# Kernel tuning notes

Measured on AMD Instinct MI355X. Metric: run time of the kernel, lower is better.

## Reference

```python
import jax, jax.numpy as jnp
import numpy as np

N, M, D = 8192, 8192, 64


def setup_inputs() -> dict:
    key = jax.random.key(0)
    kx, ky = jax.random.split(key)
    X = jax.random.normal(kx, (N, D), dtype=jnp.float32)
    Y = jax.random.normal(ky, (M, D), dtype=jnp.float32)
    return {"X": X, "Y": Y}


def reference(X, Y):
    # Pairwise Euclidean distances via the |x|^2 + |y|^2 - 2<x,y> identity
    # (avoids materializing the [N, M, D] difference tensor).
    x2 = jnp.sum(X * X, axis=1)[:, None]          # [N, 1]
    y2 = jnp.sum(Y * Y, axis=1)[None, :]          # [1, M]
    d2 = x2 + y2 - 2.0 * (X @ Y.T)                # [N, M]
    d = jnp.sqrt(jnp.maximum(d2, 0.0))            # Euclidean distance matrix
    dis_1 = jnp.mean(jnp.min(d, axis=1))          # avg over X of nearest-in-Y
    dis_2 = jnp.mean(jnp.min(d, axis=0))          # avg over Y of nearest-in-X
    return dis_1 + dis_2
```

## Files before the change

### kernel.cpp

```cpp
#include <hip/hip_runtime.h>
#include <math.h>


#define NROWS 8192
#define DDIM  64
#define CHUNKS 8
#define LSTR 72

typedef __bf16 bf16_t;
typedef bf16_t bf16x8 __attribute__((ext_vector_type(8)));
typedef float  f32x4  __attribute__((ext_vector_type(4)));


__global__ __launch_bounds__(256, 2)
void mine_kernel(const float* __restrict__ X, const float* __restrict__ Y,
                 float* __restrict__ rslab, float* __restrict__ cslab,
                 float* __restrict__ out) {
  __shared__ bf16_t Ys[128 * LSTR];
  __shared__ float y2s[128];

  const int tid = threadIdx.x;
  const int L = tid & 63;
  const int w = tid >> 6;
  const int lr = L & 15;
  const int q  = L >> 4;
  const int rh = w >> 1, ch = w & 1;
  const int itile = blockIdx.x & 63;
  const int slice = blockIdx.x >> 6;
  const int i0 = itile * 128;
  const int rgb = rh * 64, cgb = ch * 64;
  const int jbase = slice * (CHUNKS * 128);

  if (blockIdx.x == 0 && tid == 0) out[0] = 0.f;

  bf16x8 Af[8];
  float x2r[16];
  {
    float x2acc[4];
#pragma unroll
    for (int a = 0; a < 4; ++a) {
      const float4* rp = (const float4*)(X + (i0 + rgb + a * 16 + lr) * DDIM);
      float4 u0 = rp[q * 2],     u1 = rp[q * 2 + 1];
      float4 u2 = rp[8 + q * 2], u3 = rp[8 + q * 2 + 1];
      float s = 0.f;
      s = fmaf(u0.x, u0.x, s); s = fmaf(u0.y, u0.y, s);
      s = fmaf(u0.z, u0.z, s); s = fmaf(u0.w, u0.w, s);
      s = fmaf(u1.x, u1.x, s); s = fmaf(u1.y, u1.y, s);
      s = fmaf(u1.z, u1.z, s); s = fmaf(u1.w, u1.w, s);
      s = fmaf(u2.x, u2.x, s); s = fmaf(u2.y, u2.y, s);
      s = fmaf(u2.z, u2.z, s); s = fmaf(u2.w, u2.w, s);
      s = fmaf(u3.x, u3.x, s); s = fmaf(u3.y, u3.y, s);
      s = fmaf(u3.z, u3.z, s); s = fmaf(u3.w, u3.w, s);
      Af[a * 2 + 0] = (bf16x8){(bf16_t)u0.x, (bf16_t)u0.y, (bf16_t)u0.z, (bf16_t)u0.w,
                               (bf16_t)u1.x, (bf16_t)u1.y, (bf16_t)u1.z, (bf16_t)u1.w};
      Af[a * 2 + 1] = (bf16x8){(bf16_t)u2.x, (bf16_t)u2.y, (bf16_t)u2.z, (bf16_t)u2.w,
                               (bf16_t)u3.x, (bf16_t)u3.y, (bf16_t)u3.z, (bf16_t)u3.w};
      s += __shfl_xor(s, 16, 64);
      s += __shfl_xor(s, 32, 64);
      x2acc[a] = s;
    }
#pragma unroll
    for (int a = 0; a < 4; ++a)
#pragma unroll
      for (int p = 0; p < 4; ++p)
        x2r[a * 4 + p] = __shfl(x2acc[a], q * 4 + p, 64);
  }

  float rmin[16];
#pragma unroll
  for (int k = 0; k < 16; ++k) rmin[k] = INFINITY;

  for (int cc = 0; cc < CHUNKS; ++cc) {
    const int j0 = jbase + cc * 128;
    __syncthreads();
#pragma unroll
    for (int p = 0; p < 4; ++p) {
      int f = p * 256 + tid;
      int r = f >> 3, c = f & 7;
      const float4* yp = (const float4*)(Y + (j0 + r) * DDIM);
      float4 a0 = yp[c * 2], a1 = yp[c * 2 + 1];
      float s = 0.f;
      s = fmaf(a0.x, a0.x, s); s = fmaf(a0.y, a0.y, s);
      s = fmaf(a0.z, a0.z, s); s = fmaf(a0.w, a0.w, s);
      s = fmaf(a1.x, a1.x, s); s = fmaf(a1.y, a1.y, s);
      s = fmaf(a1.z, a1.z, s); s = fmaf(a1.w, a1.w, s);
      s += __shfl_xor(s, 1, 64);
      s += __shfl_xor(s, 2, 64);
      s += __shfl_xor(s, 4, 64);
      if ((tid & 7) == 0) y2s[r] = s;
      bf16x8 hv = {(bf16_t)a0.x, (bf16_t)a0.y, (bf16_t)a0.z, (bf16_t)a0.w,
                   (bf16_t)a1.x, (bf16_t)a1.y, (bf16_t)a1.z, (bf16_t)a1.w};
      *(bf16x8*)&Ys[r * LSTR + c * 8] = hv;
    }
    __syncthreads();

    float y2c[4];
#pragma unroll
    for (int b = 0; b < 4; ++b) y2c[b] = y2s[cgb + b * 16 + lr];

    f32x4 acc[4][4];
#pragma unroll
    for (int a = 0; a < 4; ++a)
#pragma unroll
      for (int b = 0; b < 4; ++b) acc[a][b] = (f32x4){0.f, 0.f, 0.f, 0.f};

#pragma unroll
    for (int b = 0; b < 4; ++b) {
      bf16x8 B0 = *(const bf16x8*)&Ys[(cgb + b * 16 + lr) * LSTR + q * 8];
      bf16x8 B1 = *(const bf16x8*)&Ys[(cgb + b * 16 + lr) * LSTR + 32 + q * 8];
#pragma unroll
      for (int a = 0; a < 4; ++a) {
        acc[a][b] = __builtin_amdgcn_mfma_f32_16x16x32_bf16(Af[a * 2 + 0], B0, acc[a][b], 0, 0, 0);
        acc[a][b] = __builtin_amdgcn_mfma_f32_16x16x32_bf16(Af[a * 2 + 1], B1, acc[a][b], 0, 0, 0);
      }
    }

    float cmin[4] = {INFINITY, INFINITY, INFINITY, INFINITY};
#pragma unroll
    for (int a = 0; a < 4; ++a)
#pragma unroll
      for (int p = 0; p < 4; ++p) {
        float x2v = x2r[a * 4 + p];
        float t0 = fmaf(-2.f, acc[a][0][p], y2c[0]);
        float t1 = fmaf(-2.f, acc[a][1][p], y2c[1]);
        float t2 = fmaf(-2.f, acc[a][2][p], y2c[2]);
        float t3 = fmaf(-2.f, acc[a][3][p], y2c[3]);
        rmin[a * 4 + p] = fminf(rmin[a * 4 + p],
                                fminf(fminf(t0, t1), fminf(t2, t3)));
        cmin[0] = fminf(cmin[0], fmaf(-2.f, acc[a][0][p], x2v));
        cmin[1] = fminf(cmin[1], fmaf(-2.f, acc[a][1][p], x2v));
        cmin[2] = fminf(cmin[2], fmaf(-2.f, acc[a][2][p], x2v));
        cmin[3] = fminf(cmin[3], fmaf(-2.f, acc[a][3][p], x2v));
      }
#pragma unroll
    for (int b = 0; b < 4; ++b) {
      cmin[b] = fminf(cmin[b], __shfl_xor(cmin[b], 16, 64));
      cmin[b] = fminf(cmin[b], __shfl_xor(cmin[b], 32, 64));
    }
    float v = cmin[0], yv = y2c[0];
    if (q == 1) { v = cmin[1]; yv = y2c[1]; }
    else if (q == 2) { v = cmin[2]; yv = y2c[2]; }
    else if (q == 3) { v = cmin[3]; yv = y2c[3]; }
    cslab[(itile * 2 + rh) * NROWS + j0 + cgb + L] = v + yv;
  }

#pragma unroll
  for (int a = 0; a < 4; ++a)
#pragma unroll
    for (int p = 0; p < 4; ++p) {
      float v = rmin[a * 4 + p];
      v = fminf(v, __shfl_xor(v, 1, 64));
      v = fminf(v, __shfl_xor(v, 2, 64));
      v = fminf(v, __shfl_xor(v, 4, 64));
      v = fminf(v, __shfl_xor(v, 8, 64));
      if (lr == 0)
        rslab[slice * (NROWS * 2) + (i0 + rgb + a * 16 + q * 4 + p) * 2 + ch] =
            v + x2r[a * 4 + p];
    }
}

__global__ void finish_kernel(const float* __restrict__ rslab,
                              const float* __restrict__ cslab,
                              float* __restrict__ out) {
  const int b = blockIdx.x;
  const int tid = threadIdx.x;
  if (b < 32) {
    int row = b * 256 + tid;
    float m = INFINITY;
#pragma unroll
    for (int g = 0; g < 8; ++g) {
      float2 v = *(const float2*)&rslab[g * (NROWS * 2) + row * 2];
      m = fminf(m, fminf(v.x, v.y));
    }
    float v = sqrtf(fmaxf(m, 0.f)) * (1.0f / 8192.0f);
#pragma unroll
    for (int off = 32; off > 0; off >>= 1) v += __shfl_down(v, off, 64);
    __shared__ float partial[4];
    if ((tid & 63) == 0) partial[tid >> 6] = v;
    __syncthreads();
    if (tid == 0)
      atomicAdd(out, partial[0] + partial[1] + partial[2] + partial[3]);
  } else {
    int j = (b - 32) * 64 + (tid & 63);
    int seg = tid >> 6;
    float m = INFINITY;
#pragma unroll
    for (int k = 0; k < 32; ++k)
      m = fminf(m, cslab[(seg * 32 + k) * NROWS + j]);
    __shared__ float red[4][64];
    red[seg][tid & 63] = m;
    __syncthreads();
    if (tid < 64) {
      float mc = fminf(fminf(red[0][tid], red[1][tid]),
                       fminf(red[2][tid], red[3][tid]));
      float v = sqrtf(fmaxf(mc, 0.f)) * (1.0f / 8192.0f);
#pragma unroll
      for (int off = 32; off > 0; off >>= 1) v += __shfl_down(v, off, 64);
      if (tid == 0) atomicAdd(out, v);
    }
  }
}

extern "C" void kernel_launch(void* const* d_in, const int* in_sizes, int n_in,
                              void* d_out, int out_size, void* d_ws, size_t ws_size,
                              hipStream_t stream) {
  const float* X = (const float*)d_in[0];
  const float* Y = (const float*)d_in[1];
  float* out = (float*)d_out;

  float* rslab = (float*)d_ws;
  float* cslab = rslab + 8 * NROWS * 2;

  mine_kernel<<<512, 256, 0, stream>>>(X, Y, rslab, cslab, out);
  finish_kernel<<<160, 256, 0, stream>>>(rslab, cslab, out);
}
```

Measured before the change: 89.27 us.

## Precompute bf16 operands and norms in a prep kernel, split Y into more slices

A new prep kernel converts X and Y to bf16 once and computes their squared norms into workspace. The main kernel then copies pre-converted bf16 tiles straight into LDS instead of converting fp32 and reducing norms on every tile. The grid grows from 512 to 2048 blocks, each handling 2 Y chunks instead of 8, with launch bounds raised to 3 blocks per CU for more parallelism. The cost is an extra kernel launch, a larger row-min slab, and more partial minima for the finish kernel to reduce.

```diff
diff --git a/kernel.cpp b/kernel.cpp
--- a/kernel.cpp
+++ b/kernel.cpp
@@ -4,20 +4,60 @@
 
 #define NROWS 8192
 #define DDIM  64
-#define CHUNKS 8
+#define ITILES 64
+#define SLICES 32
+#define CHUNKS 2
 #define LSTR 72
 
 typedef __bf16 bf16_t;
 typedef bf16_t bf16x8 __attribute__((ext_vector_type(8)));
+typedef bf16_t bf16x4 __attribute__((ext_vector_type(4)));
 typedef float  f32x4  __attribute__((ext_vector_type(4)));
 
 
-__global__ __launch_bounds__(256, 2)
-void mine_kernel(const float* __restrict__ X, const float* __restrict__ Y,
-                 float* __restrict__ rslab, float* __restrict__ cslab,
-                 float* __restrict__ out) {
+__global__ void prep_kernel(const float* __restrict__ X,
+                            const float* __restrict__ Y,
+                            bf16_t* __restrict__ Xbf, bf16_t* __restrict__ Ybf,
+                            float* __restrict__ x2, float* __restrict__ y2,
+                            float* __restrict__ out) {
+  int t = blockIdx.x * blockDim.x + threadIdx.x;
+  int half = t >> 15;
+  int r = (t >> 2) & (NROWS - 1);
+  int part = t & 3;
+  const float* src = half ? Y : X;
+  bf16_t* dst = half ? Ybf : Xbf;
+  float* sq = half ? y2 : x2;
+
+  const float4* p = (const float4*)(src + r * DDIM + part * 16);
+  float4 v0 = p[0], v1 = p[1], v2 = p[2], v3 = p[3];
+  float s = 0.f;
+  s = fmaf(v0.x, v0.x, s); s = fmaf(v0.y, v0.y, s);
+  s = fmaf(v0.z, v0.z, s); s = fmaf(v0.w, v0.w, s);
+  s = fmaf(v1.x, v1.x, s); s = fmaf(v1.y, v1.y, s);
+  s = fmaf(v1.z, v1.z, s); s = fmaf(v1.w, v1.w, s);
+  s = fmaf(v2.x, v2.x, s); s = fmaf(v2.y, v2.y, s);
+  s = fmaf(v2.z, v2.z, s); s = fmaf(v2.w, v2.w, s);
+  s = fmaf(v3.x, v3.x, s); s = fmaf(v3.y, v3.y, s);
+  s = fmaf(v3.z, v3.z, s); s = fmaf(v3.w, v3.w, s);
+
+  bf16x8 h0 = {(bf16_t)v0.x, (bf16_t)v0.y, (bf16_t)v0.z, (bf16_t)v0.w,
+               (bf16_t)v1.x, (bf16_t)v1.y, (bf16_t)v1.z, (bf16_t)v1.w};
+  bf16x8 h1 = {(bf16_t)v2.x, (bf16_t)v2.y, (bf16_t)v2.z, (bf16_t)v2.w,
+               (bf16_t)v3.x, (bf16_t)v3.y, (bf16_t)v3.z, (bf16_t)v3.w};
+  *(bf16x8*)&dst[r * DDIM + part * 16] = h0;
+  *(bf16x8*)&dst[r * DDIM + part * 16 + 8] = h1;
+
+  s += __shfl_xor(s, 1, 64);
+  s += __shfl_xor(s, 2, 64);
+  if (part == 0) sq[r] = s;
+  if (t == 0) out[0] = 0.f;
+}
+
+__global__ __launch_bounds__(256, 3)
+void mine_kernel(const bf16_t* __restrict__ Xbf, const bf16_t* __restrict__ Ybf,
+                 const float* __restrict__ x2g, const float* __restrict__ y2g,
+                 float* __restrict__ rslab, float* __restrict__ cslab) {
   __shared__ bf16_t Ys[128 * LSTR];
-  __shared__ float y2s[128];
 
   const int tid = threadIdx.x;
   const int L = tid & 63;
@@ -25,46 +65,23 @@
   const int lr = L & 15;
   const int q  = L >> 4;
   const int rh = w >> 1, ch = w & 1;
-  const int itile = blockIdx.x & 63;
+  const int itile = blockIdx.x & (ITILES - 1);
   const int slice = blockIdx.x >> 6;
   const int i0 = itile * 128;
   const int rgb = rh * 64, cgb = ch * 64;
   const int jbase = slice * (CHUNKS * 128);
 
-  if (blockIdx.x == 0 && tid == 0) out[0] = 0.f;
-
   bf16x8 Af[8];
-  float x2r[16];
-  {
-    float x2acc[4];
-#pragma unroll
-    for (int a = 0; a < 4; ++a) {
-      const float4* rp = (const float4*)(X + (i0 + rgb + a * 16 + lr) * DDIM);
-      float4 u0 = rp[q * 2],     u1 = rp[q * 2 + 1];
-      float4 u2 = rp[8 + q * 2], u3 = rp[8 + q * 2 + 1];
-      float s = 0.f;
-      s = fmaf(u0.x, u0.x, s); s = fmaf(u0.y, u0.y, s);
-      s = fmaf(u0.z, u0.z, s); s = fmaf(u0.w, u0.w, s);
-      s = fmaf(u1.x, u1.x, s); s = fmaf(u1.y, u1.y, s);
-      s = fmaf(u1.z, u1.z, s); s = fmaf(u1.w, u1.w, s);
-      s = fmaf(u2.x, u2.x, s); s = fmaf(u2.y, u2.y, s);
-      s = fmaf(u2.z, u2.z, s); s = fmaf(u2.w, u2.w, s);
-      s = fmaf(u3.x, u3.x, s); s = fmaf(u3.y, u3.y, s);
-      s = fmaf(u3.z, u3.z, s); s = fmaf(u3.w, u3.w, s);
-      Af[a * 2 + 0] = (bf16x8){(bf16_t)u0.x, (bf16_t)u0.y, (bf16_t)u0.z, (bf16_t)u0.w,
-                               (bf16_t)u1.x, (bf16_t)u1.y, (bf16_t)u1.z, (bf16_t)u1.w};
-      Af[a * 2 + 1] = (bf16x8){(bf16_t)u2.x, (bf16_t)u2.y, (bf16_t)u2.z, (bf16_t)u2.w,
-                               (bf16_t)u3.x, (bf16_t)u3.y, (bf16_t)u3.z, (bf16_t)u3.w};
-      s += __shfl_xor(s, 16, 64);
-      s += __shfl_xor(s, 32, 64);
-      x2acc[a] = s;
-    }
-#pragma unroll
-    for (int a = 0; a < 4; ++a)
-#pragma unroll
-      for (int p = 0; p < 4; ++p)
-        x2r[a * 4 + p] = __shfl(x2acc[a], q * 4 + p, 64);
+#pragma unroll
+  for (int a = 0; a < 4; ++a) {
+    int row = i0 + rgb + a * 16 + lr;
+#pragma unroll
+    for (int h = 0; h < 2; ++h)
+      Af[a * 2 + h] = *(const bf16x8*)&Xbf[row * DDIM + h * 32 + q * 8];
   }
+  float x2acc[4];
+#pragma unroll
+  for (int a = 0; a < 4; ++a) x2acc[a] = x2g[i0 + rgb + a * 16 + lr];
 
   float rmin[16];
 #pragma unroll
@@ -72,31 +89,17 @@
 
   for (int cc = 0; cc < CHUNKS; ++cc) {
     const int j0 = jbase + cc * 128;
-    __syncthreads();
+    if (cc) __syncthreads();
 #pragma unroll
     for (int p = 0; p < 4; ++p) {
       int f = p * 256 + tid;
       int r = f >> 3, c = f & 7;
-      const float4* yp = (const float4*)(Y + (j0 + r) * DDIM);
-      float4 a0 = yp[c * 2], a1 = yp[c * 2 + 1];
-      float s = 0.f;
-      s = fmaf(a0.x, a0.x, s); s = fmaf(a0.y, a0.y, s);
-      s = fmaf(a0.z, a0.z, s); s = fmaf(a0.w, a0.w, s);
-      s = fmaf(a1.x, a1.x, s); s = fmaf(a1.y, a1.y, s);
-      s = fmaf(a1.z, a1.z, s); s = fmaf(a1.w, a1.w, s);
-      s += __shfl_xor(s, 1, 64);
-      s += __shfl_xor(s, 2, 64);
-      s += __shfl_xor(s, 4, 64);
-      if ((tid & 7) == 0) y2s[r] = s;
-      bf16x8 hv = {(bf16_t)a0.x, (bf16_t)a0.y, (bf16_t)a0.z, (bf16_t)a0.w,
-                   (bf16_t)a1.x, (bf16_t)a1.y, (bf16_t)a1.z, (bf16_t)a1.w};
-      *(bf16x8*)&Ys[r * LSTR + c * 8] = hv;
-    }
+      *(bf16x8*)&Ys[r * LSTR + c * 8] = *(const bf16x8*)&Ybf[(j0 + r) * DDIM + c * 8];
+    }
+    float y2c[4];
+#pragma unroll
+    for (int b = 0; b < 4; ++b) y2c[b] = y2g[j0 + cgb + b * 16 + lr];
     __syncthreads();
-
-    float y2c[4];
-#pragma unroll
-    for (int b = 0; b < 4; ++b) y2c[b] = y2s[cgb + b * 16 + lr];
 
     f32x4 acc[4][4];
 #pragma unroll
@@ -120,7 +123,7 @@
     for (int a = 0; a < 4; ++a)
 #pragma unroll
       for (int p = 0; p < 4; ++p) {
-        float x2v = x2r[a * 4 + p];
+        float x2v = __shfl(x2acc[a], q * 4 + p, 64);
         float t0 = fmaf(-2.f, acc[a][0][p], y2c[0]);
         float t1 = fmaf(-2.f, acc[a][1][p], y2c[1]);
         float t2 = fmaf(-2.f, acc[a][2][p], y2c[2]);
@@ -153,9 +156,10 @@
       v = fminf(v, __shfl_xor(v, 2, 64));
       v = fminf(v, __shfl_xor(v, 4, 64));
       v = fminf(v, __shfl_xor(v, 8, 64));
+      float x2v = __shfl(x2acc[a], q * 4 + p, 64);
       if (lr == 0)
         rslab[slice * (NROWS * 2) + (i0 + rgb + a * 16 + q * 4 + p) * 2 + ch] =
-            v + x2r[a * 4 + p];
+            v + x2v;
     }
 }
 
@@ -168,7 +172,7 @@
     int row = b * 256 + tid;
     float m = INFINITY;
 #pragma unroll
-    for (int g = 0; g < 8; ++g) {
+    for (int g = 0; g < SLICES; ++g) {
       float2 v = *(const float2*)&rslab[g * (NROWS * 2) + row * 2];
       m = fminf(m, fminf(v.x, v.y));
     }
@@ -208,9 +212,15 @@
   const float* Y = (const float*)d_in[1];
   float* out = (float*)d_out;
 
-  float* rslab = (float*)d_ws;
-  float* cslab = rslab + 8 * NROWS * 2;
-
-  mine_kernel<<<512, 256, 0, stream>>>(X, Y, rslab, cslab, out);
+  char* wsb = (char*)d_ws;
+  bf16_t* Xbf = (bf16_t*)wsb;
+  bf16_t* Ybf = (bf16_t*)(wsb + (size_t)NROWS * DDIM * 2);
+  float* x2 = (float*)(wsb + 2 * (size_t)NROWS * DDIM * 2);
+  float* y2 = x2 + NROWS;
+  float* rslab = y2 + NROWS;
+  float* cslab = rslab + SLICES * NROWS * 2;
+
+  prep_kernel<<<(2 * NROWS * 4) / 256, 256, 0, stream>>>(X, Y, Xbf, Ybf, x2, y2, out);
+  mine_kernel<<<ITILES * SLICES, 256, 0, stream>>>(Xbf, Ybf, x2, y2, rslab, cslab);
   finish_kernel<<<160, 256, 0, stream>>>(rslab, cslab, out);
 }
```

Result: no change. 88.57 us (-0.8%).
